# Performance work log

Hardware: AMD Instinct MI355X
Metric: run time of the kernel (lower is better)

The kernel has to match this reference:

```python
import jax, jax.numpy as jnp
import numpy as np

N = 200      # nodes (fixed by Linear(200,100) on x.T)
E = 8000     # edges
NFEAT, NHID, NCLASS = 8192, 2048, 512


def _cheb_conv(x, edge_index, edge_weight, W, b):
    """PyG ChebConv (K=3, sym norm, lambda_max=2): L_hat = -D^{-1/2} A D^{-1/2}.
    T0 = x, T1 = L_hat x, T2 = 2 L_hat T1 - T0; out = sum_k T_k @ W[k] + b."""
    row, col = edge_index[0], edge_index[1]
    deg = jax.ops.segment_sum(edge_weight, row, num_segments=N)
    safe = jnp.where(deg > 0, deg, 1.0)
    dinv = jnp.where(deg > 0, 1.0 / jnp.sqrt(safe), 0.0)
    norm = -dinv[row] * edge_weight * dinv[col]  # [E]

    def lap(z):  # messages from source j=row to target i=col
        return jax.ops.segment_sum(norm[:, None] * z[row], col, num_segments=N)

    T1 = lap(x)
    T2 = 2.0 * lap(T1) - x
    return x @ W[0] + T1 @ W[1] + T2 @ W[2] + b


def _forward_single(x, ei, ew, W1, b1, W2, b2):
    h = jax.nn.relu(_cheb_conv(x, ei, ew, W1, b1))
    # dropout is identity in eval mode
    return _cheb_conv(h, ei, ew, W2, b2)  # [N, NCLASS]


def _classifier(z, Wc1, bc1, Wc2, bc2, Wc3, bc3):
    h = jax.nn.relu(z @ Wc1.T + bc1)
    h = jax.nn.relu(h @ Wc2.T + bc2)
    return h @ Wc3.T + bc3  # [NCLASS, 1]


def setup_inputs() -> dict:
    key = jax.random.key(0)
    ks = jax.random.split(key, 12)
    inp = {
        'x1': jax.random.normal(ks[0], (N, NFEAT), jnp.float32),
        'edge_index1': jax.random.randint(ks[1], (2, E), 0, N, jnp.int64),
        'edge_attr1': jax.random.uniform(ks[2], (E,), jnp.float32),
        'x2': jax.random.normal(ks[3], (N, NFEAT), jnp.float32),
        'edge_index2': jax.random.randint(ks[4], (2, E), 0, N, jnp.int64),
        'edge_attr2': jax.random.uniform(ks[5], (E,), jnp.float32),
        'W1': jax.random.normal(ks[6], (3, NFEAT, NHID), jnp.float32) * (NFEAT ** -0.5),
        'b1': jnp.zeros((NHID,), jnp.float32),
        'W2': jax.random.normal(ks[7], (3, NHID, NCLASS), jnp.float32) * (NHID ** -0.5),
        'b2': jnp.zeros((NCLASS,), jnp.float32),
        'Wc1': jax.random.normal(ks[8], (100, 200), jnp.float32) * (200 ** -0.5),
        'bc1': jnp.zeros((100,), jnp.float32),
        'Wc2': jax.random.normal(ks[9], (50, 100), jnp.float32) * (100 ** -0.5),
        'bc2': jnp.zeros((50,), jnp.float32),
        'Wc3': jax.random.normal(ks[10], (1, 50), jnp.float32) * (50 ** -0.5),
        'bc3': jnp.zeros((1,), jnp.float32),
    }
    return inp


def reference(x1, edge_index1, edge_attr1, x2, edge_index2, edge_attr2,
              W1, b1, W2, b2, Wc1, bc1, Wc2, bc2, Wc3, bc3):
    o1 = _forward_single(x1, edge_index1, edge_attr1, W1, b1, W2, b2)
    o2 = _forward_single(x2, edge_index2, edge_attr2, W1, b1, W2, b2)
    out1 = _classifier(o1.T, Wc1, bc1, Wc2, bc2, Wc3, bc3)  # [NCLASS, 1]
    out2 = _classifier(o2.T, Wc1, bc1, Wc2, bc2, Wc3, bc3)
    return out1, out2
```

## Files before the change

kernel.cpp:

```cpp
#include <hip/hip_runtime.h>

typedef __attribute__((ext_vector_type(8))) short short8;
typedef __attribute__((ext_vector_type(4))) float f32x4;
typedef __attribute__((ext_vector_type(2))) float f32x2;
typedef __attribute__((ext_vector_type(4))) unsigned int u32x4;

#define NNODES 200
#define NEDGE  8000
#define NF1    8192
#define NH     2048
#define NCL    512
#define K1     24576
#define K2     6144
#define MR     448
#define MV     400
#define PV     400
#define KC1    16
#define BK1    1536
#define KC2    16
#define BK2    384
#define M1T    224

#define OFF_P1  0ull
#define SZ_P1   ((unsigned long long)KC1*PV*NH*4)
#define OFF_P2  (OFF_P1 + SZ_P1)
#define SZ_P2   ((unsigned long long)KC2*PV*NCL*4)
#define OFF_A1  (OFF_P2 + SZ_P2)
#define SZ_A1   ((unsigned long long)MR*K1*2)
#define OFF_A2  (OFF_A1 + SZ_A1)
#define SZ_A2   ((unsigned long long)MR*K2*2)
#define OFF_LD  (OFF_A2 + SZ_A2)
#define OFF_LL  (OFF_LD + 320000ull)
#define OFF_Z   OFF_P1

static __device__ __forceinline__ unsigned short f2bf(float f) {
  unsigned int u = __float_as_uint(f);
  unsigned int r = (u + 0x7fffu + ((u >> 16) & 1u)) >> 16;
  return (unsigned short)r;
}
static __device__ __forceinline__ unsigned packbf(float a, float b) {
  return (unsigned)f2bf(a) | ((unsigned)f2bf(b) << 16);
}

__global__ void k_zero(f32x4* p1, int n1, f32x4* p2, int n2, f32x4* p3, int n3) {
  int i = blockIdx.x * 256 + threadIdx.x;
  f32x4 z = {0.f, 0.f, 0.f, 0.f};
  if (i < n1) p1[i] = z;
  i -= n1;
  if (i >= 0 && i < n2) p2[i] = z;
  i -= n2;
  if (i >= 0 && i < n3) p3[i] = z;
}

__global__ __launch_bounds__(1024)
void k_graph(const int* __restrict__ ei1, const float* __restrict__ ew1,
             const int* __restrict__ ei2, const float* __restrict__ ew2,
             float* __restrict__ Ld) {
  __shared__ float degs[NNODES];
  const int g = blockIdx.x;
  const int* ei = g ? ei2 : ei1;
  const float* ew = g ? ew2 : ew1;
  const int t = threadIdx.x;

  if (t < NNODES) degs[t] = 0.f;
  __syncthreads();
  for (int e = t; e < NEDGE; e += 1024) atomicAdd(&degs[ei[e]], ew[e]);
  __syncthreads();
  if (t < NNODES) {
    float d = degs[t];
    degs[t] = d > 0.f ? 1.0f / sqrtf(d) : 0.f;
  }
  __syncthreads();
  float* Lg = Ld + (size_t)g * NNODES * NNODES;
  for (int e = t; e < NEDGE; e += 1024) {
    int r = ei[e], c = ei[NEDGE + e];
    float nrm = -degs[r] * ew[e] * degs[c];
    atomicAdd(Lg + (size_t)c * NNODES + r, nrm);
  }
}

__global__ void k_LL(const float* __restrict__ Ld, unsigned short* __restrict__ LLb) {
  int b = blockIdx.x;
  int g = b / NNODES, i = b % NNODES;
  __shared__ float Lr[NNODES];
  const float* Lg = Ld + (size_t)g * NNODES * NNODES;
  int t = threadIdx.x;
  if (t < NNODES) Lr[t] = Lg[i * NNODES + t];
  __syncthreads();
  if (t < NNODES) {
    float acc = 0.f;
    for (int k = 0; k < NNODES; ++k) acc = fmaf(Lr[k], Lg[k * NNODES + t], acc);
    unsigned short* LLg = LLb + (size_t)g * MR * 224;
    LLg[(size_t)i * 224 + t] = f2bf(Lr[t]);
    LLg[(size_t)(NNODES + i) * 224 + t] = f2bf(2.f * acc - (i == t ? 1.f : 0.f));
  }
}

__global__ void k_t0(const float* __restrict__ x1, const float* __restrict__ x2,
                     unsigned short* __restrict__ A1) {
  int gid = blockIdx.x * 256 + threadIdx.x;
  int row = gid / (NF1 / 8);
  int c8 = (gid % (NF1 / 8)) * 8;
  const float* xp = (row < NNODES ? x1 + (size_t)row * NF1
                                  : x2 + (size_t)(row - NNODES) * NF1) + c8;
  f32x4 a = *(const f32x4*)xp;
  f32x4 b = *(const f32x4*)(xp + 4);
  u32x4 o;
  o[0] = packbf(a[0], a[1]);
  o[1] = packbf(a[2], a[3]);
  o[2] = packbf(b[0], b[1]);
  o[3] = packbf(b[2], b[3]);
  *(u32x4*)(A1 + (size_t)row * K1 + c8) = o;
}

__global__ __launch_bounds__(256, 1)
void k_abuild(const unsigned short* __restrict__ LLb, const unsigned short* __restrict__ Asrc,
              unsigned short* __restrict__ Adst, const int Nf, const int Ka) {
  __shared__ __align__(16) unsigned short XF[7][4][64][8];
  const int g = blockIdx.x & 1;
  const int nt = blockIdx.x >> 1;
  const int nbase = nt * 64;
  const int t = threadIdx.x;

  #pragma unroll
  for (int it = 0; it < 14; ++it) {
    const int pos = it * 256 + t;
    const int j = pos >> 4;
    const int n4 = (pos & 15) * 4;
    unsigned long long v = 0ull;
    if (j < NNODES)
      v = *(const unsigned long long*)(Asrc + (size_t)(g * NNODES + j) * Ka + nbase + n4);
    const int ks = j >> 5, kg = (j >> 3) & 3, jj = j & 7;
    #pragma unroll
    for (int e = 0; e < 4; ++e) {
      const int nn = n4 + e;
      XF[ks][nn >> 4][(nn & 15) + 16 * kg][jj] = (unsigned short)(v >> (16 * e));
    }
  }
  __syncthreads();

  const int w = t >> 6, lane = t & 63;
  const int lm = lane & 15, lk8 = (lane >> 4) * 8;
  f32x4 acc[7][4];
  #pragma unroll
  for (int i = 0; i < 7; ++i)
    #pragma unroll
    for (int j = 0; j < 4; ++j) acc[i][j] = (f32x4){0.f, 0.f, 0.f, 0.f};

  const unsigned short* LLg = LLb + (size_t)g * MR * 224;
  #pragma unroll
  for (int ks = 0; ks < 7; ++ks) {
    short8 bfr[4];
    #pragma unroll
    for (int nf = 0; nf < 4; ++nf) bfr[nf] = *(const short8*)&XF[ks][nf][lane][0];
    short8 af[7];
    #pragma unroll
    for (int mf = 0; mf < 7; ++mf)
      af[mf] = *(const short8*)(LLg + (size_t)(w * 112 + mf * 16 + lm) * 224 + ks * 32 + lk8);
    #pragma unroll
    for (int mf = 0; mf < 7; ++mf)
      #pragma unroll
      for (int nf = 0; nf < 4; ++nf)
        acc[mf][nf] = __builtin_amdgcn_mfma_f32_16x16x32_bf16(af[mf], bfr[nf], acc[mf][nf], 0, 0, 0);
  }

  const int lr4 = (lane >> 4) * 4;
  #pragma unroll
  for (int mf = 0; mf < 7; ++mf) {
    #pragma unroll
    for (int ri = 0; ri < 4; ++ri) {
      const int m = w * 112 + mf * 16 + lr4 + ri;
      if (m < MV) {
        const int drow = g * NNODES + (m < NNODES ? m : m - NNODES);
        const size_t dbase = (size_t)drow * Ka + (m < NNODES ? Nf : 2 * Nf) + nbase + lm;
        #pragma unroll
        for (int nf = 0; nf < 4; ++nf)
          Adst[dbase + nf * 16] = f2bf(acc[mf][nf][ri]);
      }
    }
  }
}

__global__ __launch_bounds__(256, 2)
void k_gemm1(const float* __restrict__ W, const unsigned short* __restrict__ A,
             float* __restrict__ P) {
  constexpr int Nn = NH;
  constexpr int BK = BK1;
  constexpr int ABUF = M1T * 128;
  __shared__ __align__(16) unsigned short Atile[2 * M1T * 64];
  __shared__ __align__(16) unsigned short Wt[8 * 1024];

  const int t = threadIdx.x;
  const int w = t >> 6, lane = t & 63;
  const int wm = w >> 1, wn = w & 1;
  const int lm = lane & 15, l4 = lane >> 4;
  const int b = blockIdx.x;
  const int kc = b & 15;
  const int m  = (b >> 4) & 1;
  const int nt = b >> 5;
  const int kbase = kc * BK;
  const int nbase = nt * 128;
  const int nks = BK >> 6;

  const int gb = ((t * 16) & 127) ^ (((t >> 3) & 7) << 4);
  const char* Ab = (const char*)A + ((size_t)(m * M1T + (t >> 3)) * K1 + kbase) * 2 + gb;
  const size_t CSTEP = (size_t)32 * K1 * 2;

  const int kk0 = (t >> 4) * 4;
  const int colb = (t & 15) * 8;
  const float* Wg = W + (size_t)(kbase + kk0) * Nn + nbase + colb;
  int offWl[2][8];
  #pragma unroll
  for (int p = 0; p < 2; ++p) {
    const int kk = kk0 + 2 * p;
    const int ks0 = kk >> 5, kg0 = (kk >> 3) & 3, jj1 = (kk & 7) >> 1;
    #pragma unroll
    for (int e = 0; e < 8; ++e) {
      const int nn = colb + e;
      const int nf = nn >> 4;
      const int ln = ((nn & 15) + 16 * kg0) ^ (nf & 3);
      offWl[p][e] = ((ks0 * 8 + nf) * 64 + ln) * 4 + jj1;
    }
  }

  const int aBase = (wm * 112 + lm) * 128 + ((l4 * 16) ^ ((lm & 7) << 4));
  int bAddr[4];
  #pragma unroll
  for (int nf = 0; nf < 4; ++nf) {
    const int nfg = wn * 4 + nf;
    bAddr[nf] = (nfg * 64 + (lane ^ (nfg & 3))) * 16;
  }

  f32x4 acc[7][4];
  #pragma unroll
  for (int i = 0; i < 7; ++i)
    #pragma unroll
    for (int j = 0; j < 4; ++j) acc[i][j] = (f32x4){0.f, 0.f, 0.f, 0.f};

  u32x4 areg[7];
  f32x4 wv[4][2];

  auto loadA = [&](int kt) {
    #pragma unroll
    for (int c = 0; c < 7; ++c)
      areg[c] = *(const u32x4*)(Ab + c * CSTEP + (size_t)kt * 128);
  };
  auto loadW = [&](int kt) {
    const float* p = Wg + (size_t)kt * 64 * Nn;
    #pragma unroll
    for (int r = 0; r < 4; ++r) {
      wv[r][0] = __builtin_nontemporal_load((const f32x4*)(p + (size_t)r * Nn));
      wv[r][1] = __builtin_nontemporal_load((const f32x4*)(p + (size_t)r * Nn + 4));
    }
  };
  auto storeA = [&](int buf) {
    #pragma unroll
    for (int c = 0; c < 7; ++c)
      *(u32x4*)((char*)Atile + buf * ABUF + c * 4096 + t * 16) = areg[c];
  };
  auto storeW = [&]() {
    unsigned* w32 = (unsigned*)Wt;
    #pragma unroll
    for (int p = 0; p < 2; ++p)
      #pragma unroll
      for (int e = 0; e < 8; ++e)
        w32[offWl[p][e]] = packbf(wv[2 * p][e >> 2][e & 3], wv[2 * p + 1][e >> 2][e & 3]);
  };
  auto compute = [&](int buf, int ks) {
    short8 bfr[4];
    #pragma unroll
    for (int nf = 0; nf < 4; ++nf)
      bfr[nf] = *(const short8*)((const char*)Wt + bAddr[nf] + ks * 8192);
    short8 af[7];
    #pragma unroll
    for (int mf = 0; mf < 7; ++mf)
      af[mf] = *(const short8*)((const char*)Atile + buf * ABUF + ((aBase + mf * 2048) ^ (ks * 64)));
    #pragma unroll
    for (int mf = 0; mf < 7; ++mf)
      #pragma unroll
      for (int nf = 0; nf < 4; ++nf)
        acc[mf][nf] = __builtin_amdgcn_mfma_f32_16x16x32_bf16(af[mf], bfr[nf], acc[mf][nf], 0, 0, 0);
  };

  loadA(0);
  loadW(0);
  storeA(0);
  storeW();
  __syncthreads();

  for (int kt = 0; kt < nks; ++kt) {
    const int buf = kt & 1;
    const bool more = (kt + 1 < nks);
    if (more) { loadA(kt + 1); loadW(kt + 1); }
    compute(buf, 0);
    compute(buf, 1);
    if (more) {
      storeA(buf ^ 1);
      __syncthreads();
      storeW();
      __syncthreads();
    }
  }

  float* Pk = P + ((size_t)kc * PV) * Nn + nbase;
  #pragma unroll
  for (int mf = 0; mf < 7; ++mf) {
    const int row0 = m * M1T + wm * 112 + mf * 16 + l4 * 4;
    #pragma unroll
    for (int ri = 0; ri < 4; ++ri) {
      const int row = row0 + ri;
      if (row < MV) {
        #pragma unroll
        for (int nf = 0; nf < 4; ++nf) {
          const int col = (wn * 4 + nf) * 16 + lm;
          __builtin_nontemporal_store(acc[mf][nf][ri], Pk + (size_t)row * Nn + col);
        }
      }
    }
  }
}

template <int BN, int KA, int KC>
__global__ __launch_bounds__(512, 2)
void k_gemm(const float* __restrict__ W, const unsigned short* __restrict__ A,
            float* __restrict__ P, const int Nn, const int BK) {
  constexpr int NF = BN / 16;
  constexpr int NFW = BN / 32;
  constexpr int CW = BN / 16;
  constexpr int ABUF = MR * 128;
  constexpr int BSTRIDE = NF * 1024;
  constexpr int WBUF = 2 * BSTRIDE;
  __shared__ __align__(16) unsigned short Atile[2 * MR * 64];
  __shared__ __align__(16) unsigned short Wt[2 * NF * 1024];

  const int t = threadIdx.x;
  const int w = t >> 6, lane = t & 63;
  const int wm = w >> 1, wn = w & 1;
  const int lm = lane & 15;
  const int l4 = lane >> 4;
  const int kc = blockIdx.x % KC;
  const int nt = blockIdx.x / KC;
  const int kbase = kc * BK;
  const int nbase = nt * BN;
  const int nks = BK >> 6;

  const int arow0 = t >> 3;
  const int agb = ((t * 16) & 127) ^ ((arow0 & 7) << 4);
  const char* Ab = (const char*)A + (size_t)kbase * 2 + (size_t)arow0 * (KA * 2) + agb;
  const size_t CSTEP = (size_t)64 * KA * 2;

  const int kk0 = (t >> 4) * 2;
  const int colb = (t & 15) * CW;
  const float* Wg = W + (size_t)(kbase + kk0) * Nn + nbase + colb;
  int offWl[CW];
  {
    const int ks0 = kk0 >> 5, kg0 = (kk0 >> 3) & 3, jj1 = (kk0 & 7) >> 1;
    #pragma unroll
    for (int e = 0; e < CW; ++e) {
      const int nn = colb + e;
      const int nf = nn >> 4;
      const int ln = ((nn & 15) + 16 * kg0) ^ (nf & 3);
      offWl[e] = ((ks0 * NF + nf) * 64 + ln) * 4 + jj1;
    }
  }

  const int aBase = (wm * 112 + lm) * 128 + ((l4 * 16) ^ ((lm & 7) << 4));
  int bAddr[NFW];
  #pragma unroll
  for (int nf = 0; nf < NFW; ++nf) {
    const int nfg = wn * NFW + nf;
    bAddr[nf] = nfg * 1024 + (lane ^ (nfg & 3)) * 16;
  }

  f32x4 acc[7][NFW];
  #pragma unroll
  for (int i = 0; i < 7; ++i)
    #pragma unroll
    for (int j = 0; j < NFW; ++j) acc[i][j] = (f32x4){0.f, 0.f, 0.f, 0.f};

  u32x4 areg[7];
  f32x2 w0s, w1s;

  auto loadW = [&](int kt) {
    const float* p = Wg + (size_t)kt * 64 * Nn;
    w0s = __builtin_nontemporal_load((const f32x2*)p);
    w1s = __builtin_nontemporal_load((const f32x2*)(p + Nn));
  };
  auto loadA = [&](int kt) {
    #pragma unroll
    for (int c = 0; c < 7; ++c)
      areg[c] = *(const u32x4*)(Ab + c * CSTEP + (size_t)kt * 128);
  };
  auto storeA = [&](int buf) {
    #pragma unroll
    for (int c = 0; c < 7; ++c)
      *(u32x4*)((char*)Atile + buf * ABUF + c * 8192 + t * 16) = areg[c];
  };
  auto storeW = [&](int buf) {
    unsigned* w32 = (unsigned*)Wt + buf * (WBUF / 4);
    #pragma unroll
    for (int e = 0; e < CW; ++e)
      w32[offWl[e]] = packbf(w0s[e & 1], w1s[e & 1]);
  };

  loadW(0);
  loadA(0);
  storeA(0);
  storeW(0);
  __syncthreads();

  for (int kt = 0; kt < nks; ++kt) {
    const int buf = kt & 1;
    const bool more = (kt + 1 < nks);
    if (more) loadW(kt + 1);

    #pragma unroll
    for (int ks = 0; ks < 2; ++ks) {
      short8 bfr[NFW];
      #pragma unroll
      for (int nf = 0; nf < NFW; ++nf)
        bfr[nf] = *(const short8*)((const char*)Wt + buf * WBUF + bAddr[nf] + ks * BSTRIDE);
      const int abx = (aBase ^ (ks * 64)) + buf * ABUF;
      short8 af[7];
      #pragma unroll
      for (int mf = 0; mf < 7; ++mf)
        af[mf] = *(const short8*)((const char*)Atile + abx + mf * 2048);
      #pragma unroll
      for (int mf = 0; mf < 7; ++mf)
        #pragma unroll
        for (int nf = 0; nf < NFW; ++nf)
          acc[mf][nf] = __builtin_amdgcn_mfma_f32_16x16x32_bf16(af[mf], bfr[nf], acc[mf][nf], 0, 0, 0);
      if (ks == 0 && more) loadA(kt + 1);
    }

    if (more) {
      storeA(buf ^ 1);
      storeW(buf ^ 1);
    }
    __syncthreads();
  }

  float* Pk = P + ((size_t)kc * PV) * Nn + nbase;
  #pragma unroll
  for (int mf = 0; mf < 7; ++mf) {
    const int row0 = wm * 112 + mf * 16 + l4 * 4;
    #pragma unroll
    for (int ri = 0; ri < 4; ++ri) {
      const int row = row0 + ri;
      if (row < MV) {
        #pragma unroll
        for (int nf = 0; nf < NFW; ++nf) {
          const int col = (wn * NFW + nf) * 16 + lm;
          __builtin_nontemporal_store(acc[mf][nf][ri], Pk + (size_t)row * Nn + col);
        }
      }
    }
  }
}

__global__ void k_ep1(const float* __restrict__ P1, const float* __restrict__ b1,
                      unsigned short* __restrict__ A2) {
  int gid = blockIdx.x * 256 + threadIdx.x;
  int row = gid / (NH / 4);
  int c = (gid % (NH / 4)) * 4;
  f32x4 s = {0.f, 0.f, 0.f, 0.f};
  #pragma unroll
  for (int kc = 0; kc < KC1; ++kc)
    s += __builtin_nontemporal_load((const f32x4*)(P1 + ((size_t)kc * PV + row) * NH + c));
  const f32x4 b = *(const f32x4*)(b1 + c);
  unsigned long long pack = 0;
  #pragma unroll
  for (int i = 0; i < 4; ++i) {
    float v = s[i] + b[i];
    pack |= (unsigned long long)f2bf(v > 0.f ? v : 0.f) << (16 * i);
  }
  *(unsigned long long*)(A2 + (size_t)row * K2 + c) = pack;
}

__global__ __launch_bounds__(256)
void k_zsum(const float* __restrict__ P2, const float* __restrict__ b2,
            float* __restrict__ zt) {
  __shared__ float tile[8][264];
  const int b = blockIdx.x;
  const int g = b / 50;
  const int r2 = b % 50;
  const int j0 = (r2 >> 1) * 8;
  const int ch = (r2 & 1) * 256;
  const int t = threadIdx.x;
  const int j = t >> 5;
  const int c0 = (t & 31) * 8;
  const int row = g * NNODES + j0 + j;

  #pragma unroll
  for (int ci = 0; ci < 2; ++ci) {
    const int c = c0 + ci * 4;
    f32x4 s = *(const f32x4*)(b2 + ch + c);
    #pragma unroll
    for (int kc = 0; kc < KC2; ++kc)
      s += __builtin_nontemporal_load((const f32x4*)(P2 + ((size_t)kc * PV + row) * NCL + ch + c));
    *(f32x4*)&tile[j][c] = s;
  }
  __syncthreads();

  f32x4 lo, hi;
  #pragma unroll
  for (int e = 0; e < 4; ++e) { lo[e] = tile[e][t]; hi[e] = tile[4 + e][t]; }
  float* zr = zt + ((size_t)g * NCL + ch + t) * 200 + j0;
  *(f32x4*)zr = lo;
  *(f32x4*)(zr + 4) = hi;
}

__global__ __launch_bounds__(256)
void k_cls2(const float* __restrict__ zt,
            const float* __restrict__ Wc1, const float* __restrict__ bc1,
            const float* __restrict__ Wc2, const float* __restrict__ bc2,
            const float* __restrict__ Wc3, const float* __restrict__ bc3,
            float* __restrict__ outp) {
  __shared__ float W1s[100 * 201];
  __shared__ float W2s[50 * 101];
  __shared__ float zs[4][200];
  __shared__ float h1s[4][104];
  __shared__ float h2s[4][56];
  const int g = blockIdx.x >> 7;
  const int t = threadIdx.x;
  const int w = t >> 6, lane = t & 63;
  const int r = (blockIdx.x & 127) * 4 + w;

  for (int i = t; i < 20000; i += 256) {
    const int c = i / 200, j = i - c * 200;
    W1s[c * 201 + j] = Wc1[i];
  }
  for (int i = t; i < 5000; i += 256) {
    const int c = i / 100, j = i - c * 100;
    W2s[c * 101 + j] = Wc2[i];
  }
  const float* zr = zt + ((size_t)g * NCL + r) * 200;
  #pragma unroll
  for (int i = 0; i < 4; ++i) {
    const int idx = i * 64 + lane;
    if (idx < 200) zs[w][idx] = zr[idx];
  }
  __syncthreads();

  {
    const int c1 = lane + 64;
    const int c1m = (c1 < 100) ? c1 : 99;
    float a0 = bc1[lane];
    float a1 = bc1[c1m];
    #pragma unroll 4
    for (int j = 0; j < 200; ++j) {
      const float zv = zs[w][j];
      a0 = fmaf(zv, W1s[lane * 201 + j], a0);
      a1 = fmaf(zv, W1s[c1m * 201 + j], a1);
    }
    h1s[w][lane] = a0 > 0.f ? a0 : 0.f;
    if (c1 < 100) h1s[w][c1] = a1 > 0.f ? a1 : 0.f;
  }
  __syncthreads();

  {
    const int c2 = (lane < 50) ? lane : 49;
    float b = bc2[c2];
    #pragma unroll 4
    for (int c = 0; c < 100; ++c) b = fmaf(h1s[w][c], W2s[c2 * 101 + c], b);
    if (lane < 50) h2s[w][lane] = b > 0.f ? b : 0.f;
  }
  __syncthreads();

  {
    float v = (lane < 50) ? h2s[w][lane] * Wc3[lane] : 0.f;
    #pragma unroll
    for (int off = 32; off >= 1; off >>= 1) v += __shfl_down(v, off);
    if (lane == 0) outp[g * NCL + r] = v + bc3[0];
  }
}

extern "C" void kernel_launch(void* const* d_in, const int* in_sizes, int n_in,
                              void* d_out, int out_size, void* d_ws, size_t ws_size,
                              hipStream_t stream) {
  const float* x1  = (const float*)d_in[0];
  const int*   ei1 = (const int*)d_in[1];
  const float* ea1 = (const float*)d_in[2];
  const float* x2  = (const float*)d_in[3];
  const int*   ei2 = (const int*)d_in[4];
  const float* ea2 = (const float*)d_in[5];
  const float* W1  = (const float*)d_in[6];
  const float* b1  = (const float*)d_in[7];
  const float* W2  = (const float*)d_in[8];
  const float* b2  = (const float*)d_in[9];
  const float* Wc1 = (const float*)d_in[10];
  const float* bc1 = (const float*)d_in[11];
  const float* Wc2 = (const float*)d_in[12];
  const float* bc2 = (const float*)d_in[13];
  const float* Wc3 = (const float*)d_in[14];
  const float* bc3 = (const float*)d_in[15];
  float* outp = (float*)d_out;

  char* ws = (char*)d_ws;
  float*          P1  = (float*)(ws + OFF_P1);
  float*          P2  = (float*)(ws + OFF_P2);
  unsigned short* A1  = (unsigned short*)(ws + OFF_A1);
  unsigned short* A2  = (unsigned short*)(ws + OFF_A2);
  float*          Ld  = (float*)(ws + OFF_LD);
  unsigned short* LLb = (unsigned short*)(ws + OFF_LL);
  float*          zt  = (float*)(ws + OFF_Z);

  k_zero<<<897, 256, 0, stream>>>(
      (f32x4*)(ws + OFF_LD), 45088,
      (f32x4*)(ws + OFF_A1 + (size_t)MV * K1 * 2), 147456,
      (f32x4*)(ws + OFF_A2 + (size_t)MV * K2 * 2), 36864);

  k_graph<<<2, 1024, 0, stream>>>(ei1, ea1, ei2, ea2, Ld);
  k_LL<<<400, 256, 0, stream>>>(Ld, LLb);
  k_t0<<<1600, 256, 0, stream>>>(x1, x2, A1);
  k_abuild<<<(NF1 / 64) * 2, 256, 0, stream>>>(LLb, A1, A1, NF1, K1);
  k_gemm1<<<512, 256, 0, stream>>>(W1, A1, P1);
  k_ep1<<<800, 256, 0, stream>>>(P1, b1, A2);
  k_abuild<<<(NH / 64) * 2, 256, 0, stream>>>(LLb, A2, A2, NH, K2);
  k_gemm<32, K2, KC2><<<KC2 * (NCL / 32), 512, 0, stream>>>(W2, A2, P2, NCL, BK2);
  k_zsum<<<100, 256, 0, stream>>>(P2, b2, zt);
  k_cls2<<<256, 256, 0, stream>>>(zt, Wc1, bc1, Wc2, bc2, Wc3, bc3, outp);
}
```

Measured before the change: 219.6 us.

## Halve gemm1 N-tile, double-buffer W tile, and drop one barrier per step

Narrows the first big GEMM's output tile from 128 to 64 columns, which doubles the grid to 1024 blocks and halves the per-thread W loads and accumulators. The W shared tile is now double-buffered, so each k-step needs one barrier instead of two, and the A global loads are moved between the two compute halves to overlap them with MFMA work. The cost is that each A tile is loaded twice as often across blocks (less reuse of A per block) and there are fewer MFMAs per LDS read of A.

```diff
diff --git a/kernel.cpp b/kernel.cpp
--- a/kernel.cpp
+++ b/kernel.cpp
@@ -186,9 +186,13 @@
              float* __restrict__ P) {
   constexpr int Nn = NH;
   constexpr int BK = BK1;
+  constexpr int NF = 4;
+  constexpr int NFW = 2;
   constexpr int ABUF = M1T * 128;
+  constexpr int BSTRIDE = NF * 1024;
+  constexpr int WBUF = 2 * BSTRIDE;
   __shared__ __align__(16) unsigned short Atile[2 * M1T * 64];
-  __shared__ __align__(16) unsigned short Wt[8 * 1024];
+  __shared__ __align__(16) unsigned short Wt[2 * NF * 1024];
 
   const int t = threadIdx.x;
   const int w = t >> 6, lane = t & 63;
@@ -199,7 +203,7 @@
   const int m  = (b >> 4) & 1;
   const int nt = b >> 5;
   const int kbase = kc * BK;
-  const int nbase = nt * 128;
+  const int nbase = nt * 64;
   const int nks = BK >> 6;
 
   const int gb = ((t * 16) & 127) ^ (((t >> 3) & 7) << 4);
@@ -207,70 +211,68 @@
   const size_t CSTEP = (size_t)32 * K1 * 2;
 
   const int kk0 = (t >> 4) * 4;
-  const int colb = (t & 15) * 8;
+  const int colb = (t & 15) * 4;
   const float* Wg = W + (size_t)(kbase + kk0) * Nn + nbase + colb;
-  int offWl[2][8];
+  int offWl[2][4];
   #pragma unroll
   for (int p = 0; p < 2; ++p) {
     const int kk = kk0 + 2 * p;
     const int ks0 = kk >> 5, kg0 = (kk >> 3) & 3, jj1 = (kk & 7) >> 1;
     #pragma unroll
-    for (int e = 0; e < 8; ++e) {
+    for (int e = 0; e < 4; ++e) {
       const int nn = colb + e;
       const int nf = nn >> 4;
       const int ln = ((nn & 15) + 16 * kg0) ^ (nf & 3);
-      offWl[p][e] = ((ks0 * 8 + nf) * 64 + ln) * 4 + jj1;
+      offWl[p][e] = ((ks0 * NF + nf) * 64 + ln) * 4 + jj1;
     }
   }
 
   const int aBase = (wm * 112 + lm) * 128 + ((l4 * 16) ^ ((lm & 7) << 4));
-  int bAddr[4];
-  #pragma unroll
-  for (int nf = 0; nf < 4; ++nf) {
-    const int nfg = wn * 4 + nf;
-    bAddr[nf] = (nfg * 64 + (lane ^ (nfg & 3))) * 16;
-  }
-
-  f32x4 acc[7][4];
+  int bAddr[NFW];
+  #pragma unroll
+  for (int nf = 0; nf < NFW; ++nf) {
+    const int nfg = wn * NFW + nf;
+    bAddr[nf] = nfg * 1024 + (lane ^ (nfg & 3)) * 16;
+  }
+
+  f32x4 acc[7][NFW];
   #pragma unroll
   for (int i = 0; i < 7; ++i)
     #pragma unroll
-    for (int j = 0; j < 4; ++j) acc[i][j] = (f32x4){0.f, 0.f, 0.f, 0.f};
+    for (int j = 0; j < NFW; ++j) acc[i][j] = (f32x4){0.f, 0.f, 0.f, 0.f};
 
   u32x4 areg[7];
-  f32x4 wv[4][2];
-
+  f32x4 wv[4];
+
+  auto loadW = [&](int kt) {
+    const float* p = Wg + (size_t)kt * 64 * Nn;
+    #pragma unroll
+    for (int r = 0; r < 4; ++r)
+      wv[r] = __builtin_nontemporal_load((const f32x4*)(p + (size_t)r * Nn));
+  };
   auto loadA = [&](int kt) {
     #pragma unroll
     for (int c = 0; c < 7; ++c)
       areg[c] = *(const u32x4*)(Ab + c * CSTEP + (size_t)kt * 128);
   };
-  auto loadW = [&](int kt) {
-    const float* p = Wg + (size_t)kt * 64 * Nn;
-    #pragma unroll
-    for (int r = 0; r < 4; ++r) {
-      wv[r][0] = __builtin_nontemporal_load((const f32x4*)(p + (size_t)r * Nn));
-      wv[r][1] = __builtin_nontemporal_load((const f32x4*)(p + (size_t)r * Nn + 4));
-    }
-  };
   auto storeA = [&](int buf) {
     #pragma unroll
     for (int c = 0; c < 7; ++c)
       *(u32x4*)((char*)Atile + buf * ABUF + c * 4096 + t * 16) = areg[c];
   };
-  auto storeW = [&]() {
-    unsigned* w32 = (unsigned*)Wt;
+  auto storeW = [&](int buf) {
+    unsigned* w32 = (unsigned*)Wt + buf * (WBUF / 4);
     #pragma unroll
     for (int p = 0; p < 2; ++p)
       #pragma unroll
-      for (int e = 0; e < 8; ++e)
-        w32[offWl[p][e]] = packbf(wv[2 * p][e >> 2][e & 3], wv[2 * p + 1][e >> 2][e & 3]);
+      for (int e = 0; e < 4; ++e)
+        w32[offWl[p][e]] = packbf(wv[2 * p][e], wv[2 * p + 1][e]);
   };
   auto compute = [&](int buf, int ks) {
-    short8 bfr[4];
-    #pragma unroll
-    for (int nf = 0; nf < 4; ++nf)
-      bfr[nf] = *(const short8*)((const char*)Wt + bAddr[nf] + ks * 8192);
+    short8 bfr[NFW];
+    #pragma unroll
+    for (int nf = 0; nf < NFW; ++nf)
+      bfr[nf] = *(const short8*)((const char*)Wt + buf * WBUF + bAddr[nf] + ks * BSTRIDE);
     short8 af[7];
     #pragma unroll
     for (int mf = 0; mf < 7; ++mf)
@@ -278,28 +280,28 @@
     #pragma unroll
     for (int mf = 0; mf < 7; ++mf)
       #pragma unroll
-      for (int nf = 0; nf < 4; ++nf)
+      for (int nf = 0; nf < NFW; ++nf)
         acc[mf][nf] = __builtin_amdgcn_mfma_f32_16x16x32_bf16(af[mf], bfr[nf], acc[mf][nf], 0, 0, 0);
   };
 
+  loadW(0);
   loadA(0);
-  loadW(0);
   storeA(0);
-  storeW();
+  storeW(0);
   __syncthreads();
 
   for (int kt = 0; kt < nks; ++kt) {
     const int buf = kt & 1;
     const bool more = (kt + 1 < nks);
-    if (more) { loadA(kt + 1); loadW(kt + 1); }
+    if (more) loadW(kt + 1);
     compute(buf, 0);
+    if (more) loadA(kt + 1);
     compute(buf, 1);
     if (more) {
       storeA(buf ^ 1);
-      __syncthreads();
-      storeW();
-      __syncthreads();
-    }
+      storeW(buf ^ 1);
+    }
+    __syncthreads();
   }
 
   float* Pk = P + ((size_t)kc * PV) * Nn + nbase;
@@ -311,8 +313,8 @@
       const int row = row0 + ri;
       if (row < MV) {
         #pragma unroll
-        for (int nf = 0; nf < 4; ++nf) {
-          const int col = (wn * 4 + nf) * 16 + lm;
+        for (int nf = 0; nf < NFW; ++nf) {
+          const int col = (wn * NFW + nf) * 16 + lm;
           __builtin_nontemporal_store(acc[mf][nf][ri], Pk + (size_t)row * Nn + col);
         }
       }
@@ -614,7 +616,7 @@
   k_LL<<<400, 256, 0, stream>>>(Ld, LLb);
   k_t0<<<1600, 256, 0, stream>>>(x1, x2, A1);
   k_abuild<<<(NF1 / 64) * 2, 256, 0, stream>>>(LLb, A1, A1, NF1, K1);
-  k_gemm1<<<512, 256, 0, stream>>>(W1, A1, P1);
+  k_gemm1<<<1024, 256, 0, stream>>>(W1, A1, P1);
   k_ep1<<<800, 256, 0, stream>>>(P1, b1, A2);
   k_abuild<<<(NH / 64) * 2, 256, 0, stream>>>(LLb, A2, A2, NH, K2);
   k_gemm<32, K2, KC2><<<KC2 * (NCL / 32), 512, 0, stream>>>(W2, A2, P2, NCL, BK2);
```

Measured after the change: 212.8 us. -3.1%, faster.
